# Optimization experiments

Hardware: AMD Instinct MI355X
Metric: run time of the kernel (lower is better)

Reference implementation:

```python
import jax, jax.numpy as jnp
import numpy as np
import math

CHUNK = 128


def setup_inputs() -> dict:
    key = jax.random.key(0)
    ks = jax.random.split(key, 12)
    B, S, H, D = 2, 4096, 1024, 2048  # D = hidden_dim * expansion_factor
    std = 0.02
    inp = {
        "hidden_states": jax.random.normal(ks[0], (B, S, H), jnp.float32),
        "Wq": jax.random.normal(ks[1], (H, D), jnp.float32) * std,
        "bq": jnp.zeros((D,), jnp.float32),
        "Wk": jax.random.normal(ks[2], (H, D), jnp.float32) * std,
        "bk": jnp.zeros((D,), jnp.float32),
        "Wv": jax.random.normal(ks[3], (H, D), jnp.float32) * std,
        "bv": jnp.zeros((D,), jnp.float32),
        "Wg": jax.random.normal(ks[4], (H, D), jnp.float32) * std,
        "bg": jnp.zeros((D,), jnp.float32),
        "Wo": jax.random.normal(ks[5], (D, H), jnp.float32) * std,
        "bo": jnp.zeros((H,), jnp.float32),
    }
    return inp


def reference(hidden_states, Wq, bq, Wk, bk, Wv, bv, Wg, bg, Wo, bo):
    B, S, H = hidden_states.shape
    D = Wq.shape[1]
    cs = CHUNK
    nC = S // cs  # seq_len chosen as multiple of chunk_size (no padding path)

    q = hidden_states @ Wq + bq
    k = hidden_states @ Wk + bk
    v = hidden_states @ Wv + bv
    gate = jax.nn.sigmoid(hidden_states @ Wg + bg)

    qc = q.reshape(B, nC, cs, D)
    kc = k.reshape(B, nC, cs, D)
    vc = v.reshape(B, nC, cs, D)
    gc = gate.reshape(B, nC, cs, D)

    # intra-chunk causal softmax attention (vectorized over all chunks)
    scale = 1.0 / math.sqrt(D)
    attn = jnp.einsum('bncd,bnkd->bnck', qc, kc) * scale  # [B,nC,cs,cs]
    causal = jnp.tril(jnp.ones((cs, cs), bool))
    attn = jnp.where(causal, attn, -jnp.inf)
    attn = jax.nn.softmax(attn, axis=-1)
    local = jnp.einsum('bnck,bnkd->bncd', attn, vc)

    # inter-chunk linear-attention state accumulation:
    # cross_i = q_i @ sum_{j<i} K_j^T V_j  (sequential scan over chunks)
    def step(state, xs):
        qi, ki, vi = xs  # each [B,cs,D]
        cross = jnp.einsum('bcd,bde->bce', qi, state)
        state = state + jnp.einsum('bcd,bce->bde', ki, vi)
        return state, cross

    state0 = jnp.zeros((B, D, D), hidden_states.dtype)
    _, cross = jax.lax.scan(
        step, state0,
        (qc.transpose(1, 0, 2, 3), kc.transpose(1, 0, 2, 3), vc.transpose(1, 0, 2, 3)))
    cross = cross.transpose(1, 0, 2, 3)  # [B,nC,cs,D]

    out = (local + cross) * gc
    out = out.reshape(B, S, D)
    return out @ Wo + bo
```

## Files before the change

kernel.cpp:

```cpp
#include <hip/hip_runtime.h>
#include <hip/hip_bf16.h>
#include <math.h>


typedef __bf16 bf16_t;
typedef __bf16 bf16x8 __attribute__((ext_vector_type(8)));
typedef __bf16 bf16x4 __attribute__((ext_vector_type(4)));
typedef float f32x4 __attribute__((ext_vector_type(4)));

#define NB_ 2
#define SEQ 4096
#define HID 1024
#define DD 2048
#define BS 8192
#define LDS_CORE 131072
#define SP 264

__device__ __forceinline__ void async16(const void* g, void* l) {
  __builtin_amdgcn_global_load_lds(
      (const __attribute__((address_space(1))) void*)g,
      (__attribute__((address_space(3))) void*)l, 16, 0, 0);
}

#define VMW4 asm volatile("s_waitcnt vmcnt(4)" ::: "memory")
#define VMW0 asm volatile("s_waitcnt vmcnt(0)" ::: "memory")
#define BARR __builtin_amdgcn_s_barrier()
#define FEN asm volatile("" ::: "memory")

__device__ __forceinline__ void core256(const bf16_t* __restrict__ A, int lda,
                                        const bf16_t* __restrict__ B, int ldb, int nt,
                                        bf16_t* lds, f32x4 (&acc)[8][4]) {
  constexpr int UE = 16384;
  constexpr int BUFE = 32768;
  const int t = threadIdx.x, lane = t & 63, w = t >> 6;
  const int wm = w >> 2, wn = w & 3;
  const int lr = lane & 15, lg = lane >> 4;
  const int sw8 = (lg ^ (lr & 3)) * 8;
  int aOff[8], bOff[4];
#pragma unroll
  for (int f = 0; f < 8; ++f) aOff[f] = (wm * 128 + f * 16 + lr) * 32 + sw8;
#pragma unroll
  for (int n = 0; n < 4; ++n) bOff[n] = 8192 + (wn * 64 + n * 16 + lr) * 32 + sw8;
  const int ssl = ((t & 3) ^ ((t >> 2) & 3)) * 8;
  const int r0 = t >> 2;
  const int srcA0 = r0 * lda + ssl, srcA1 = (128 + r0) * lda + ssl;
  const int srcB0 = r0 * ldb + ssl, srcB1 = (128 + r0) * ldb + ssl;
  const int dstT = t * 8;

#pragma unroll
  for (int m = 0; m < 8; ++m)
#pragma unroll
    for (int n = 0; n < 4; ++n) acc[m][n] = (f32x4){0.f, 0.f, 0.f, 0.f};

#define ISSUE_UNIT(Ak, Bk, buf, h)                       \
  {                                                      \
    bf16_t* u_ = (buf) + (h)*UE;                         \
    const bf16_t* a_ = (Ak) + (h)*32;                    \
    const bf16_t* b_ = (Bk) + (h)*32;                    \
    async16(a_ + srcA0, u_ + dstT);                      \
    async16(a_ + srcA1, u_ + 4096 + dstT);               \
    async16(b_ + srcB0, u_ + 8192 + dstT);               \
    async16(b_ + srcB1, u_ + 12288 + dstT);              \
  }

  ISSUE_UNIT(A, B, lds, 0);
  ISSUE_UNIT(A, B, lds, 1);

  for (int tt = 0; tt < nt; ++tt) {
    bf16_t* cur = lds + (tt & 1) * BUFE;
    bf16_t* nxt = lds + ((tt + 1) & 1) * BUFE;
    const int kb = (tt + 1 < nt ? tt + 1 : 0) << 6;
    const bf16_t* An = A + kb;
    const bf16_t* Bn = B + kb;
#pragma unroll
    for (int h = 0; h < 2; ++h) {
      VMW4; BARR; FEN;
      const bf16_t* u = cur + h * UE;
      bf16x8 af[8], bv[4];
#pragma unroll
      for (int f = 0; f < 8; ++f) af[f] = *reinterpret_cast<const bf16x8*>(&u[aOff[f]]);
#pragma unroll
      for (int n = 0; n < 4; ++n) bv[n] = *reinterpret_cast<const bf16x8*>(&u[bOff[n]]);
      ISSUE_UNIT(An, Bn, nxt, h);
      __builtin_amdgcn_s_setprio(1);
#pragma unroll
      for (int mf = 0; mf < 8; ++mf)
#pragma unroll
        for (int nf = 0; nf < 4; ++nf)
          acc[mf][nf] = __builtin_amdgcn_mfma_f32_16x16x32_bf16(af[mf], bv[nf],
                                                                acc[mf][nf], 0, 0, 0);
      __builtin_amdgcn_s_setprio(0);
    }
  }
  VMW0; BARR; FEN;
#undef ISSUE_UNIT
}

__global__ void k_cvt(const float4* __restrict__ in, bf16x4* __restrict__ out, int n4) {
  int i = blockIdx.x * blockDim.x + threadIdx.x;
  if (i < n4) {
    float4 v = in[i];
    bf16x4 o;
    o[0] = (bf16_t)v.x; o[1] = (bf16_t)v.y; o[2] = (bf16_t)v.z; o[3] = (bf16_t)v.w;
    out[i] = o;
  }
}

__global__ void k_tconv(const float* __restrict__ in, bf16_t* __restrict__ out,
                        int R, int C) {
  __shared__ bf16_t tile[64][65];
  int bc = blockIdx.x, br = blockIdx.y;
  int t = threadIdx.x;
  int c = t & 63, r0 = t >> 6;
#pragma unroll
  for (int rr = 0; rr < 64; rr += 4) {
    int r = rr + r0;
    tile[r][c] = (bf16_t)in[(long)(br * 64 + r) * C + bc * 64 + c];
  }
  __syncthreads();
#pragma unroll
  for (int rr = 0; rr < 64; rr += 4) {
    int r = rr + r0;
    out[(long)(bc * 64 + r) * R + br * 64 + c] = tile[c][r];
  }
}

__global__ __launch_bounds__(512, 1) void k_gemm_qkvg(
    const bf16_t* __restrict__ hsb, const bf16_t* __restrict__ Wt4,
    const float* __restrict__ bq, const float* __restrict__ bk,
    const float* __restrict__ bv, const float* __restrict__ bg,
    bf16_t* __restrict__ out, bf16_t* __restrict__ Vt) {
  extern __shared__ bf16_t lds[];
  int i = blockIdx.x;
  int xcd = i & 7, j = i >> 3;
  int nb = xcd * 4 + (j & 3);
  int mb = j >> 2;
  f32x4 acc[8][4];
  core256(hsb + (long)mb * 256 * HID, HID, Wt4 + (long)nb * 256 * HID, HID,
          HID / 64, lds, acc);
  const int t = threadIdx.x, lane = t & 63, w = t >> 6;
  const int wm = w >> 2, wn = w & 3, lr = lane & 15, lg = lane >> 4;
  int z = nb >> 3;
  const float* bias = z == 0 ? bq : z == 1 ? bk : z == 2 ? bv : bg;
  int colT = (nb & 7) * 256;
  float b4[4];
#pragma unroll
  for (int nf = 0; nf < 4; ++nf) b4[nf] = bias[colT + wn * 64 + nf * 16 + lr];
#pragma unroll
  for (int rh = 0; rh < 2; ++rh) {
    if (wm == rh) {
#pragma unroll
      for (int mf = 0; mf < 8; ++mf)
#pragma unroll
        for (int reg = 0; reg < 4; ++reg) {
          int lrow = mf * 16 + lg * 4 + reg;
#pragma unroll
          for (int nf = 0; nf < 4; ++nf) {
            float v = acc[mf][nf][reg] + b4[nf];
            if (z == 3) v = 1.f / (1.f + __expf(-v));
            lds[lrow * SP + wn * 64 + nf * 16 + lr] = (bf16_t)v;
          }
        }
    }
    __syncthreads();
    if (z != 2) {
      bf16_t* O = out + (long)z * BS * DD + ((long)mb * 256 + rh * 128) * DD + colT;
#pragma unroll
      for (int it = 0; it < 8; ++it) {
        int s = it * 512 + t;
        int row = s >> 5, sg = s & 31;
        bf16x8 v = *reinterpret_cast<const bf16x8*>(&lds[row * SP + sg * 8]);
        *reinterpret_cast<bf16x8*>(&O[(long)row * DD + sg * 8]) = v;
      }
    } else {
      int bz = mb >> 4, smb = mb & 15;
      bf16_t* Vd = Vt + ((long)bz * DD + colT) * SEQ + smb * 256 + rh * 128;
#pragma unroll
      for (int it = 0; it < 8; ++it) {
        int idx = it * 512 + t;
        int d = idx >> 4, sg = idx & 15;
        bf16x8 v;
#pragma unroll
        for (int jj = 0; jj < 8; ++jj) v[jj] = lds[(sg * 8 + jj) * SP + d];
        *reinterpret_cast<bf16x8*>(&Vd[(long)d * SEQ + sg * 8]) = v;
      }
    }
    __syncthreads();
  }
}

__global__ __launch_bounds__(512, 1) void k_pair(const bf16_t* __restrict__ Q,
                                                 const bf16_t* __restrict__ Kb,
                                                 bf16_t* __restrict__ P) {
  extern __shared__ bf16_t lds[];
  int p = blockIdx.x, b = blockIdx.y;
  int m = 0, base = 0;
  while (base + m + 1 <= p) { base += m + 1; ++m; }
  int jt = p - base;
  f32x4 acc[8][4];
  core256(Q + ((long)b * SEQ + (long)m * 256) * DD, DD,
          Kb + ((long)b * SEQ + (long)jt * 256) * DD, DD, DD / 64, lds, acc);
  const int t = threadIdx.x, lane = t & 63, w = t >> 6;
  const int wm = w >> 2, wn = w & 3, lr = lane & 15, lg = lane >> 4;
  const bool diag = (jt == m);
  const float scale = 0.02209708691207961f;
  bf16_t* Pt = P + ((long)b * SEQ + (long)m * 256) * (long)SEQ + (long)jt * 256;
#pragma unroll
  for (int rh = 0; rh < 2; ++rh) {
    if (wm == rh) {
#pragma unroll
      for (int mf = 0; mf < 8; ++mf)
#pragma unroll
        for (int reg = 0; reg < 4; ++reg) {
          int lrow = mf * 16 + lg * 4 + reg;
#pragma unroll
          for (int nf = 0; nf < 4; ++nf) {
            int col = wn * 64 + nf * 16 + lr;
            float v = acc[mf][nf][reg];
            if (diag) {
              int ch = col >> 7, c2 = col & 127;
              if (ch == rh) v = (c2 <= lrow) ? v * scale : -1e30f;
              else if (rh == 0) v = 0.f;
            }
            lds[lrow * SP + col] = (bf16_t)v;
          }
        }
    }
    __syncthreads();
    if (diag) {
      if (t < 128) {
        bf16_t* rowp = lds + t * SP + rh * 128;
        float mx = -1e30f;
        for (int cc = 0; cc <= t; ++cc) mx = fmaxf(mx, (float)rowp[cc]);
        float ssum = 0.f;
        for (int cc = 0; cc <= t; ++cc) ssum += __expf((float)rowp[cc] - mx);
        float inv = 1.f / ssum;
        for (int cc = 0; cc < 128; ++cc) {
          float v = (cc <= t) ? __expf((float)rowp[cc] - mx) * inv : 0.f;
          rowp[cc] = (bf16_t)v;
        }
      }
      __syncthreads();
    }
    bf16_t* Po = Pt + (long)rh * 128 * SEQ;
#pragma unroll
    for (int it = 0; it < 8; ++it) {
      int s = it * 512 + t;
      int row = s >> 5, sg = s & 31;
      bf16x8 v = *reinterpret_cast<const bf16x8*>(&lds[row * SP + sg * 8]);
      *reinterpret_cast<bf16x8*>(&Po[(long)row * SEQ + sg * 8]) = v;
    }
    __syncthreads();
  }
}

__global__ __launch_bounds__(512, 1) void k_gemm2(const bf16_t* __restrict__ P,
                                                  const bf16_t* __restrict__ Vt,
                                                  const bf16_t* __restrict__ G,
                                                  bf16_t* __restrict__ OutPre) {
  extern __shared__ bf16_t lds[];
  int bid = blockIdx.x;
  int ip = 15 - (bid >> 4);
  int nb = (bid >> 1) & 7, b2 = bid & 1;
  f32x4 acc[8][4];
  core256(P + ((long)b2 * SEQ + (long)ip * 256) * (long)SEQ, SEQ,
          Vt + (long)b2 * DD * SEQ + (long)nb * 256 * SEQ, SEQ, (ip + 1) * 4,
          lds, acc);
  const int t = threadIdx.x, lane = t & 63, w = t >> 6;
  const int wm = w >> 2, wn = w & 3, lr = lane & 15, lg = lane >> 4;
  long rowb = (long)b2 * SEQ + (long)ip * 256;
  int colT = nb * 256;
#pragma unroll
  for (int rh = 0; rh < 2; ++rh) {
    if (wm == rh) {
#pragma unroll
      for (int mf = 0; mf < 8; ++mf)
#pragma unroll
        for (int reg = 0; reg < 4; ++reg) {
          int lrow = mf * 16 + lg * 4 + reg;
#pragma unroll
          for (int nf = 0; nf < 4; ++nf)
            lds[lrow * SP + wn * 64 + nf * 16 + lr] = (bf16_t)acc[mf][nf][reg];
        }
    }
    __syncthreads();
    bf16_t* O = OutPre + (rowb + rh * 128) * DD + colT;
    const bf16_t* Gp = G + (rowb + rh * 128) * DD + colT;
#pragma unroll
    for (int it = 0; it < 8; ++it) {
      int s = it * 512 + t;
      int row = s >> 5, sg = s & 31;
      bf16x8 v = *reinterpret_cast<const bf16x8*>(&lds[row * SP + sg * 8]);
      bf16x8 gv = *reinterpret_cast<const bf16x8*>(&Gp[(long)row * DD + sg * 8]);
      bf16x8 o;
#pragma unroll
      for (int jj = 0; jj < 8; ++jj) o[jj] = (bf16_t)((float)v[jj] * (float)gv[jj]);
      *reinterpret_cast<bf16x8*>(&O[(long)row * DD + sg * 8]) = o;
    }
    __syncthreads();
  }
}

__global__ __launch_bounds__(512, 1) void k_gemm3(const bf16_t* __restrict__ OutPre,
                                                  const bf16_t* __restrict__ Wot,
                                                  const float* __restrict__ bo,
                                                  float* __restrict__ out) {
  extern __shared__ bf16_t lds[];
  int mb = blockIdx.x >> 2, nb = blockIdx.x & 3;
  f32x4 acc[8][4];
  core256(OutPre + (long)mb * 256 * DD, DD, Wot + (long)nb * 256 * DD, DD,
          DD / 64, lds, acc);
  const int t = threadIdx.x, lane = t & 63, w = t >> 6;
  const int wm = w >> 2, wn = w & 3, lr = lane & 15, lg = lane >> 4;
  int colbase = nb * 256 + wn * 64;
  float b4[4];
#pragma unroll
  for (int nf = 0; nf < 4; ++nf) b4[nf] = bo[colbase + nf * 16 + lr];
#pragma unroll
  for (int mf = 0; mf < 8; ++mf)
#pragma unroll
    for (int reg = 0; reg < 4; ++reg) {
      long row = mb * 256 + wm * 128 + mf * 16 + lg * 4 + reg;
#pragma unroll
      for (int nf = 0; nf < 4; ++nf)
        out[row * HID + colbase + nf * 16 + lr] = acc[mf][nf][reg] + b4[nf];
    }
}

extern "C" void kernel_launch(void* const* d_in, const int* in_sizes, int n_in,
                              void* d_out, int out_size, void* d_ws, size_t ws_size,
                              hipStream_t stream) {
  const float* hs = (const float*)d_in[0];
  const float* Wq = (const float*)d_in[1];
  const float* bq = (const float*)d_in[2];
  const float* Wk = (const float*)d_in[3];
  const float* bk = (const float*)d_in[4];
  const float* Wv = (const float*)d_in[5];
  const float* bv = (const float*)d_in[6];
  const float* Wg = (const float*)d_in[7];
  const float* bg = (const float*)d_in[8];
  const float* Wo = (const float*)d_in[9];
  const float* bo = (const float*)d_in[10];
  float* out = (float*)d_out;

  char* ws = (char*)d_ws;
  const size_t MB = 1024 * 1024;
  bf16_t* P = (bf16_t*)(ws);
  bf16_t* hsb = (bf16_t*)(ws);
  bf16_t* Wt4 = (bf16_t*)(ws + 16 * MB);
  bf16_t* Wot = (bf16_t*)(ws + 64 * MB);
  bf16_t* QKVG = (bf16_t*)(ws + 68 * MB);
  bf16_t* Vt = (bf16_t*)(ws + 196 * MB);

  bf16_t* Qb = QKVG;
  bf16_t* Kbuf = QKVG + (long)BS * DD;
  bf16_t* Vbuf = QKVG + 2l * BS * DD;
  bf16_t* Gbuf = QKVG + 3l * BS * DD;
  bf16_t* OutPre = Vbuf;

  hipFuncSetAttribute((const void*)k_gemm_qkvg,
                      hipFuncAttributeMaxDynamicSharedMemorySize, LDS_CORE);
  hipFuncSetAttribute((const void*)k_pair,
                      hipFuncAttributeMaxDynamicSharedMemorySize, LDS_CORE);
  hipFuncSetAttribute((const void*)k_gemm2,
                      hipFuncAttributeMaxDynamicSharedMemorySize, LDS_CORE);
  hipFuncSetAttribute((const void*)k_gemm3,
                      hipFuncAttributeMaxDynamicSharedMemorySize, LDS_CORE);

  k_cvt<<<(BS * HID / 4 + 255) / 256, 256, 0, stream>>>((const float4*)hs,
                                                        (bf16x4*)hsb, BS * HID / 4);
  k_tconv<<<dim3(DD / 64, HID / 64), 256, 0, stream>>>(Wq, Wt4 + 0l * DD * HID, HID, DD);
  k_tconv<<<dim3(DD / 64, HID / 64), 256, 0, stream>>>(Wk, Wt4 + 1l * DD * HID, HID, DD);
  k_tconv<<<dim3(DD / 64, HID / 64), 256, 0, stream>>>(Wv, Wt4 + 2l * DD * HID, HID, DD);
  k_tconv<<<dim3(DD / 64, HID / 64), 256, 0, stream>>>(Wg, Wt4 + 3l * DD * HID, HID, DD);
  k_tconv<<<dim3(HID / 64, DD / 64), 256, 0, stream>>>(Wo, Wot, DD, HID);

  k_gemm_qkvg<<<1024, 512, LDS_CORE, stream>>>(hsb, Wt4, bq, bk, bv, bg, QKVG, Vt);

  k_pair<<<dim3(136, 2), 512, LDS_CORE, stream>>>(Qb, Kbuf, P);

  k_gemm2<<<256, 512, LDS_CORE, stream>>>(P, Vt, Gbuf, OutPre);

  k_gemm3<<<128, 512, LDS_CORE, stream>>>(OutPre, Wot, bo, out);
}
```

Before: 525.5 us.

## Restructure GEMM core into four-phase interleaved K-64 pipeline with two blocks per CU

Reworks the shared 256x256 GEMM core so each 64-wide K tile is loaded as a single swizzled unit (8-way XOR swizzle on 64-element rows). The tile is consumed in four MFMA phases, and the async global-to-LDS loads for the next tile are spread across those phases with finer vmcnt waits and barriers. This is meant to overlap memory traffic with compute more evenly and hold fewer fragment registers at once. It also raises launch bounds to 2 blocks per CU, which caps registers per thread and may cause spills. A second resident block would also need LDS to fit, which depends on the 128KB dynamic allocation.

```diff
diff --git a/kernel.cpp b/kernel.cpp
--- a/kernel.cpp
+++ b/kernel.cpp
@@ -22,78 +22,120 @@
       (__attribute__((address_space(3))) void*)l, 16, 0, 0);
 }
 
-#define VMW4 asm volatile("s_waitcnt vmcnt(4)" ::: "memory")
-#define VMW0 asm volatile("s_waitcnt vmcnt(0)" ::: "memory")
+#define VMW(n) asm volatile("s_waitcnt vmcnt(" #n ")" ::: "memory")
 #define BARR __builtin_amdgcn_s_barrier()
 #define FEN asm volatile("" ::: "memory")
+#define LDV(p) (*reinterpret_cast<const bf16x8*>(p))
 
 __device__ __forceinline__ void core256(const bf16_t* __restrict__ A, int lda,
                                         const bf16_t* __restrict__ B, int ldb, int nt,
                                         bf16_t* lds, f32x4 (&acc)[8][4]) {
-  constexpr int UE = 16384;
-  constexpr int BUFE = 32768;
   const int t = threadIdx.x, lane = t & 63, w = t >> 6;
   const int wm = w >> 2, wn = w & 3;
   const int lr = lane & 15, lg = lane >> 4;
-  const int sw8 = (lg ^ (lr & 3)) * 8;
-  int aOff[8], bOff[4];
-#pragma unroll
-  for (int f = 0; f < 8; ++f) aOff[f] = (wm * 128 + f * 16 + lr) * 32 + sw8;
-#pragma unroll
-  for (int n = 0; n < 4; ++n) bOff[n] = 8192 + (wn * 64 + n * 16 + lr) * 32 + sw8;
-  const int ssl = ((t & 3) ^ ((t >> 2) & 3)) * 8;
-  const int r0 = t >> 2;
-  const int srcA0 = r0 * lda + ssl, srcA1 = (128 + r0) * lda + ssl;
-  const int srcB0 = r0 * ldb + ssl, srcB1 = (128 + r0) * ldb + ssl;
+  const int x7 = lr & 7;
+  const int s0 = (lg ^ x7) * 8;
+  const int s1 = ((4 + lg) ^ x7) * 8;
+  int arL[4], arH[4], brr[4];
+#pragma unroll
+  for (int f = 0; f < 4; ++f) {
+    arL[f] = (wm * 128 + f * 16 + lr) * 64;
+    arH[f] = arL[f] + 64 * 64;
+    brr[f] = 16384 + (wn * 64 + f * 16 + lr) * 64;
+  }
+  const int slog = ((t & 7) ^ ((t >> 3) & 7)) * 8;
+  const int tr = t >> 3;
+  int srcA[4], srcB[4];
+#pragma unroll
+  for (int q = 0; q < 4; ++q) {
+    srcA[q] = (q * 64 + tr) * lda + slog;
+    srcB[q] = (q * 64 + tr) * ldb + slog;
+  }
   const int dstT = t * 8;
-
 #pragma unroll
   for (int m = 0; m < 8; ++m)
 #pragma unroll
     for (int n = 0; n < 4; ++n) acc[m][n] = (f32x4){0.f, 0.f, 0.f, 0.f};
 
-#define ISSUE_UNIT(Ak, Bk, buf, h)                       \
-  {                                                      \
-    bf16_t* u_ = (buf) + (h)*UE;                         \
-    const bf16_t* a_ = (Ak) + (h)*32;                    \
-    const bf16_t* b_ = (Bk) + (h)*32;                    \
-    async16(a_ + srcA0, u_ + dstT);                      \
-    async16(a_ + srcA1, u_ + 4096 + dstT);               \
-    async16(b_ + srcB0, u_ + 8192 + dstT);               \
-    async16(b_ + srcB1, u_ + 12288 + dstT);              \
-  }
-
-  ISSUE_UNIT(A, B, lds, 0);
-  ISSUE_UNIT(A, B, lds, 1);
+  async16(B + srcB[0], lds + 16384 + dstT);
+  async16(B + srcB[1], lds + 16384 + 4096 + dstT);
+  async16(B + srcB[2], lds + 16384 + 8192 + dstT);
+  async16(B + srcB[3], lds + 16384 + 12288 + dstT);
+  async16(A + srcA[0], lds + dstT);
+  async16(A + srcA[2], lds + 8192 + dstT);
+  async16(A + srcA[1], lds + 4096 + dstT);
+  async16(A + srcA[3], lds + 12288 + dstT);
 
   for (int tt = 0; tt < nt; ++tt) {
-    bf16_t* cur = lds + (tt & 1) * BUFE;
-    bf16_t* nxt = lds + ((tt + 1) & 1) * BUFE;
+    bf16_t* cur = lds + (tt & 1) * 32768;
+    bf16_t* nxt = lds + ((tt + 1) & 1) * 32768;
     const int kb = (tt + 1 < nt ? tt + 1 : 0) << 6;
     const bf16_t* An = A + kb;
     const bf16_t* Bn = B + kb;
-#pragma unroll
-    for (int h = 0; h < 2; ++h) {
-      VMW4; BARR; FEN;
-      const bf16_t* u = cur + h * UE;
-      bf16x8 af[8], bv[4];
-#pragma unroll
-      for (int f = 0; f < 8; ++f) af[f] = *reinterpret_cast<const bf16x8*>(&u[aOff[f]]);
-#pragma unroll
-      for (int n = 0; n < 4; ++n) bv[n] = *reinterpret_cast<const bf16x8*>(&u[bOff[n]]);
-      ISSUE_UNIT(An, Bn, nxt, h);
-      __builtin_amdgcn_s_setprio(1);
-#pragma unroll
-      for (int mf = 0; mf < 8; ++mf)
-#pragma unroll
-        for (int nf = 0; nf < 4; ++nf)
-          acc[mf][nf] = __builtin_amdgcn_mfma_f32_16x16x32_bf16(af[mf], bv[nf],
-                                                                acc[mf][nf], 0, 0, 0);
-      __builtin_amdgcn_s_setprio(0);
-    }
-  }
-  VMW0; BARR; FEN;
-#undef ISSUE_UNIT
+    bf16x8 afl0[4], afh0[4], afl1[4], afh1[4], bv0[4], bv1[4];
+    VMW(2); FEN;
+    BARR; FEN;
+#pragma unroll
+    for (int f = 0; f < 4; ++f) afl0[f] = LDV(&cur[arL[f] + s0]);
+#pragma unroll
+    for (int n = 0; n < 4; ++n) bv0[n] = LDV(&cur[brr[n] + s0]);
+    async16(Bn + srcB[0], nxt + 16384 + dstT);
+    async16(Bn + srcB[1], nxt + 16384 + 4096 + dstT);
+    __builtin_amdgcn_s_setprio(1);
+#pragma unroll
+    for (int mf = 0; mf < 4; ++mf)
+#pragma unroll
+      for (int nf = 0; nf < 4; ++nf)
+        acc[mf][nf] =
+            __builtin_amdgcn_mfma_f32_16x16x32_bf16(afl0[mf], bv0[nf], acc[mf][nf], 0, 0, 0);
+    __builtin_amdgcn_s_setprio(0);
+    BARR; FEN;
+    VMW(2); FEN;
+    BARR; FEN;
+#pragma unroll
+    for (int f = 0; f < 4; ++f) afh0[f] = LDV(&cur[arH[f] + s0]);
+#pragma unroll
+    for (int f = 0; f < 4; ++f) afl1[f] = LDV(&cur[arL[f] + s1]);
+#pragma unroll
+    for (int n = 0; n < 4; ++n) bv1[n] = LDV(&cur[brr[n] + s1]);
+    async16(Bn + srcB[2], nxt + 16384 + 8192 + dstT);
+    async16(Bn + srcB[3], nxt + 16384 + 12288 + dstT);
+    __builtin_amdgcn_s_setprio(1);
+#pragma unroll
+    for (int mf = 0; mf < 4; ++mf)
+#pragma unroll
+      for (int nf = 0; nf < 4; ++nf)
+        acc[4 + mf][nf] =
+            __builtin_amdgcn_mfma_f32_16x16x32_bf16(afh0[mf], bv0[nf], acc[4 + mf][nf], 0, 0, 0);
+    __builtin_amdgcn_s_setprio(0);
+    BARR; FEN;
+#pragma unroll
+    for (int f = 0; f < 4; ++f) afh1[f] = LDV(&cur[arH[f] + s1]);
+    async16(An + srcA[0], nxt + dstT);
+    async16(An + srcA[2], nxt + 8192 + dstT);
+    __builtin_amdgcn_s_setprio(1);
+#pragma unroll
+    for (int mf = 0; mf < 4; ++mf)
+#pragma unroll
+      for (int nf = 0; nf < 4; ++nf)
+        acc[mf][nf] =
+            __builtin_amdgcn_mfma_f32_16x16x32_bf16(afl1[mf], bv1[nf], acc[mf][nf], 0, 0, 0);
+    __builtin_amdgcn_s_setprio(0);
+    BARR; FEN;
+    async16(An + srcA[1], nxt + 4096 + dstT);
+    async16(An + srcA[3], nxt + 12288 + dstT);
+    __builtin_amdgcn_s_setprio(1);
+#pragma unroll
+    for (int mf = 0; mf < 4; ++mf)
+#pragma unroll
+      for (int nf = 0; nf < 4; ++nf)
+        acc[4 + mf][nf] =
+            __builtin_amdgcn_mfma_f32_16x16x32_bf16(afh1[mf], bv1[nf], acc[4 + mf][nf], 0, 0, 0);
+    __builtin_amdgcn_s_setprio(0);
+    BARR; FEN;
+  }
+  VMW(0); FEN;
+  BARR; FEN;
 }
 
 __global__ void k_cvt(const float4* __restrict__ in, bf16x4* __restrict__ out, int n4) {
@@ -125,7 +167,7 @@
   }
 }
 
-__global__ __launch_bounds__(512, 1) void k_gemm_qkvg(
+__global__ __launch_bounds__(512, 2) void k_gemm_qkvg(
     const bf16_t* __restrict__ hsb, const bf16_t* __restrict__ Wt4,
     const float* __restrict__ bq, const float* __restrict__ bk,
     const float* __restrict__ bv, const float* __restrict__ bg,
@@ -189,7 +231,7 @@
   }
 }
 
-__global__ __launch_bounds__(512, 1) void k_pair(const bf16_t* __restrict__ Q,
+__global__ __launch_bounds__(512, 2) void k_pair(const bf16_t* __restrict__ Q,
                                                  const bf16_t* __restrict__ Kb,
                                                  bf16_t* __restrict__ P) {
   extern __shared__ bf16_t lds[];
@@ -254,7 +296,7 @@
   }
 }
 
-__global__ __launch_bounds__(512, 1) void k_gemm2(const bf16_t* __restrict__ P,
+__global__ __launch_bounds__(512, 2) void k_gemm2(const bf16_t* __restrict__ P,
                                                   const bf16_t* __restrict__ Vt,
                                                   const bf16_t* __restrict__ G,
                                                   bf16_t* __restrict__ OutPre) {
@@ -301,7 +343,7 @@
   }
 }
 
-__global__ __launch_bounds__(512, 1) void k_gemm3(const bf16_t* __restrict__ OutPre,
+__global__ __launch_bounds__(512, 2) void k_gemm3(const bf16_t* __restrict__ OutPre,
                                                   const bf16_t* __restrict__ Wot,
                                                   const float* __restrict__ bo,
                                                   float* __restrict__ out) {
```

Result: faster. 492.4 us (-6.3%).
